# Kernel optimization log

Hardware: AMD Instinct MI355X
Metric: run time of the kernel (lower is better)

The kernel has to match this reference:

```python
import jax, jax.numpy as jnp
import numpy as np

T_MAX = 20
NUM_HEADS = 8
COMPLEXITY_W = 0.3
LN_EPS = 1e-5


def _layernorm(h, g, b):
    mu = jnp.mean(h, axis=-1, keepdims=True)
    var = jnp.var(h, axis=-1, keepdims=True)
    return (h - mu) / jnp.sqrt(var + LN_EPS) * g + b


def _gate_mlp(x, W1, b1, g, be, W2, b2, W3, b3):
    # Linear -> LayerNorm -> ReLU -> (Dropout=id in eval) -> Linear -> ReLU -> Linear -> Sigmoid
    h = jax.nn.relu(_layernorm(x @ W1 + b1, g, be))
    h = jax.nn.relu(h @ W2 + b2)
    return jax.nn.sigmoid(h @ W3 + b3)


def _adaptive_windows(x, p):
    S = x.shape[1]
    gate = _gate_mlp(x, p['gW1'], p['gb1'], p['gg'], p['gbe'], p['gW2'], p['gb2'], p['gW3'], p['gb3'])
    comp = _gate_mlp(x, p['cW1'], p['cb1'], p['cg'], p['cbe'], p['cW2'], p['cb2'], p['cW3'], p['cb3'])
    pos = jnp.linspace(0.8, 1.2, S, dtype=x.dtype).reshape(1, -1, 1)
    score = ((1.0 - COMPLEXITY_W) * gate + COMPLEXITY_W * comp) * pos
    T_i = jnp.clip(jnp.ceil(score[..., 0] * T_MAX), 1, T_MAX).astype(jnp.int32)  # [B,S]
    return T_i


def _spike_sum(x, T_i, alpha, beta):
    # LIF recurrence over T_MAX steps; accumulate masked spikes. x: [B,S,E]
    z = jnp.zeros_like(x)

    def step(carry, t):
        v, i, acc = carry
        active = (t < T_i).astype(x.dtype)[..., None]  # [B,S,1]
        i = alpha * i + x * active
        v = beta * v + i
        s = (v >= 1.0).astype(x.dtype)
        v = v * (1.0 - s)  # v_reset = 0
        return (v, i, acc + s * active), None

    (_, _, acc), _ = jax.lax.scan(step, (z, z, z), jnp.arange(T_MAX))
    return acc


def _forward(x, params):
    B, S, E = x.shape
    H, D = NUM_HEADS, E // NUM_HEADS
    q = x @ params['Wq']
    k = x @ params['Wk']
    v = x @ params['Wv']
    T_i = _adaptive_windows(x, params)
    q_sum = _spike_sum(q, T_i, params['alpha_q'], params['beta_q'])
    k_sum = _spike_sum(k, T_i, params['alpha_k'], params['beta_k'])
    v_mean = _spike_sum(v, T_i, params['alpha_v'], params['beta_v']) / T_MAX
    q_sum = q_sum.reshape(B, S, H, D)
    k_sum = k_sum.reshape(B, S, H, D)
    v_mean = v_mean.reshape(B, S, H, D)
    scale = D ** -0.5
    scores = jnp.einsum('bihd,bjhd->bhij', q_sum, k_sum) * scale
    w = jax.nn.softmax(scores, axis=-1)
    out = jnp.einsum('bhij,bjhd->bihd', w, v_mean).reshape(B, S, E)
    return out @ params['Wo'] + params['bo']


def setup_inputs() -> dict:
    key = jax.random.key(0)
    ks = iter(jax.random.split(key, 32))
    B, S, E = 4, 1024, 512
    f32 = jnp.float32

    def w(shape, scale=0.02):
        return jax.random.normal(next(ks), shape, dtype=f32) * scale

    inp = {
        'x': jax.random.normal(next(ks), (B, S, E), dtype=f32),
        'Wq': w((E, E)), 'Wk': w((E, E)), 'Wv': w((E, E)),
        'Wo': w((E, E)), 'bo': jnp.zeros((E,), f32),
        'gW1': w((E, 128)), 'gb1': jnp.zeros((128,), f32),
        'gg': jnp.ones((128,), f32), 'gbe': jnp.zeros((128,), f32),
        'gW2': w((128, 64)), 'gb2': jnp.zeros((64,), f32),
        'gW3': w((64, 1)), 'gb3': jnp.zeros((1,), f32),
        'cW1': w((E, 64)), 'cb1': jnp.zeros((64,), f32),
        'cg': jnp.ones((64,), f32), 'cbe': jnp.zeros((64,), f32),
        'cW2': w((64, 32)), 'cb2': jnp.zeros((32,), f32),
        'cW3': w((32, 1)), 'cb3': jnp.zeros((1,), f32),
        'alpha_q': jnp.asarray(np.exp(-1 / 5.0), f32), 'beta_q': jnp.asarray(np.exp(-1 / 20.0), f32),
        'alpha_k': jnp.asarray(np.exp(-1 / 5.0), f32), 'beta_k': jnp.asarray(np.exp(-1 / 20.0), f32),
        'alpha_v': jnp.asarray(np.exp(-1 / 5.0), f32), 'beta_v': jnp.asarray(np.exp(-1 / 20.0), f32),
    }
    return inp


def reference(x, Wq, Wk, Wv, Wo, bo,
              gW1, gb1, gg, gbe, gW2, gb2, gW3, gb3,
              cW1, cb1, cg, cbe, cW2, cb2, cW3, cb3,
              alpha_q, beta_q, alpha_k, beta_k, alpha_v, beta_v):
    params = dict(Wq=Wq, Wk=Wk, Wv=Wv, Wo=Wo, bo=bo,
                  gW1=gW1, gb1=gb1, gg=gg, gbe=gbe, gW2=gW2, gb2=gb2, gW3=gW3, gb3=gb3,
                  cW1=cW1, cb1=cb1, cg=cg, cbe=cbe, cW2=cW2, cb2=cb2, cW3=cW3, cb3=cb3,
                  alpha_q=alpha_q, beta_q=beta_q, alpha_k=alpha_k, beta_k=beta_k,
                  alpha_v=alpha_v, beta_v=beta_v)
    return _forward(x, params)
```

## Files before the change

kernel.cpp:

```cpp
#include <hip/hip_runtime.h>
#include <math.h>

#define SEQ   1024
#define EMB   512
#define NROWS 4096
#define LDP   72
#define GROWS 4

typedef __attribute__((ext_vector_type(8))) short short8;
typedef __attribute__((ext_vector_type(4))) float float4v;

__device__ __forceinline__ float bf2f(unsigned short s) {
    union { float f; unsigned u; } x; x.u = ((unsigned)s) << 16; return x.f;
}
__device__ __forceinline__ unsigned short f2bf(float f) {
    union { float f; unsigned u; } x; x.f = f;
    unsigned r = x.u + 0x7fffu + ((x.u >> 16) & 1u);
    return (unsigned short)(r >> 16);
}

__device__ __forceinline__ void split3(float x, unsigned short& h, unsigned short& m, unsigned short& l) {
    union { float f; unsigned u; } a; a.f = x;
    const unsigned rh = a.u + 0x7fffu + ((a.u >> 16) & 1u);
    h = (unsigned short)(rh >> 16);
    union { float f; unsigned u; } hf; hf.u = rh & 0xffff0000u;
    const float r1 = x - hf.f;
    a.f = r1;
    const unsigned rm = a.u + 0x7fffu + ((a.u >> 16) & 1u);
    m = (unsigned short)(rm >> 16);
    union { float f; unsigned u; } mf; mf.u = rm & 0xffff0000u;
    const float r2 = r1 - mf.f;
    l = f2bf(r2);
}

template<int H1, int H2>
__device__ __forceinline__ double gate_mlp_block(
    const double xs[GROWS][EMB], double h1[GROWS][128], double h2[GROWS][64],
    double* red, double* mu_s, double* var_s,
    const float* __restrict__ W1, const float* __restrict__ b1,
    const float* __restrict__ gam, const float* __restrict__ bet,
    const float* __restrict__ W2, const float* __restrict__ b2,
    const float* __restrict__ W3, const float* __restrict__ b3,
    int tid, int myrow)
{
    constexpr int S  = 256 / H1;
    constexpr int KS = EMB / S;

    {
        const int col = tid % H1, sk = tid / H1;
        double acc[GROWS] = {0.0, 0.0, 0.0, 0.0};
        const int kbeg = sk * KS;
        #pragma unroll 4
        for (int k = kbeg; k < kbeg + KS; ++k) {
            const double w = (double)W1[k * H1 + col];
            #pragma unroll
            for (int r = 0; r < GROWS; ++r) acc[r] += w * xs[r][k];
        }
        #pragma unroll
        for (int r = 0; r < GROWS; ++r) red[(sk * GROWS + r) * H1 + col] = acc[r];
    }
    __syncthreads();
    for (int idx = tid; idx < GROWS * H1; idx += 256) {
        const int r = idx / H1, cc = idx % H1;
        double s = 0.0;
        #pragma unroll
        for (int t = 0; t < S; ++t) s += red[(t * GROWS + r) * H1 + cc];
        h1[r][cc] = s + (double)b1[cc];
    }
    __syncthreads();

    {
        const int w = tid >> 6, l = tid & 63;
        double s = 0.0;
        for (int c = l; c < H1; c += 64) s += h1[w][c];
        #pragma unroll
        for (int off = 32; off >= 1; off >>= 1) s += __shfl_xor(s, off);
        if (l == 0) mu_s[w] = s / (double)H1;
    }
    __syncthreads();
    {
        const int w = tid >> 6, l = tid & 63;
        const double mu = mu_s[w];
        double s = 0.0;
        for (int c = l; c < H1; c += 64) { const double d = h1[w][c] - mu; s += d * d; }
        #pragma unroll
        for (int off = 32; off >= 1; off >>= 1) s += __shfl_xor(s, off);
        if (l == 0) var_s[w] = s / (double)H1;
    }
    __syncthreads();
    for (int idx = tid; idx < GROWS * H1; idx += 256) {
        const int r = idx / H1, cc = idx % H1;
        double hn = (h1[r][cc] - mu_s[r]) / sqrt(var_s[r] + 1e-5) * (double)gam[cc] + (double)bet[cc];
        h1[r][cc] = hn > 0.0 ? hn : 0.0;
    }
    __syncthreads();

    {
        const int col = tid % H2;
        const int r   = tid / H2;
        if (r < GROWS) {
            double acc = (double)b2[col];
            for (int k = 0; k < H1; ++k)
                acc += (double)W2[k * H2 + col] * h1[r][k];
            h2[r][col] = acc > 0.0 ? acc : 0.0;
        }
    }
    __syncthreads();

    {
        const int w = tid >> 6, l = tid & 63;
        double s = 0.0;
        for (int c = l; c < H2; c += 64) s += h2[w][c] * (double)W3[c];
        #pragma unroll
        for (int off = 32; off >= 1; off >>= 1) s += __shfl_xor(s, off);
        if (l == 0) mu_s[w] = s;
    }
    __syncthreads();
    double ret = 0.0;
    if (myrow >= 0) {
        const double z = mu_s[myrow] + (double)b3[0];
        ret = 1.0 / (1.0 + exp(-z));
    }
    __syncthreads();
    return ret;
}

__global__ __launch_bounds__(256) void gates_kernel(
    const float* __restrict__ x,
    const float* __restrict__ gW1, const float* __restrict__ gb1,
    const float* __restrict__ gg,  const float* __restrict__ gbe,
    const float* __restrict__ gW2, const float* __restrict__ gb2,
    const float* __restrict__ gW3, const float* __restrict__ gb3,
    const float* __restrict__ cW1, const float* __restrict__ cb1,
    const float* __restrict__ cg,  const float* __restrict__ cbe,
    const float* __restrict__ cW2, const float* __restrict__ cb2,
    const float* __restrict__ cW3, const float* __restrict__ cb3,
    int* __restrict__ T_i)
{
    __shared__ double xs[GROWS][EMB];
    __shared__ double h1[GROWS][128];
    __shared__ double h2[GROWS][64];
    __shared__ double red[1024];
    __shared__ double mu_s[GROWS], var_s[GROWS];

    const int row0 = blockIdx.x * GROWS;
    const int tid = threadIdx.x;

    for (int idx = tid; idx < GROWS * EMB; idx += 256) {
        const int r = idx >> 9, cc = idx & 511;
        xs[r][cc] = (double)x[(size_t)(row0 + r) * EMB + cc];
    }
    __syncthreads();

    const int myrow = (tid < GROWS) ? tid : -1;
    const double g0 = gate_mlp_block<128, 64>(xs, h1, h2, red, mu_s, var_s,
                                              gW1, gb1, gg, gbe, gW2, gb2, gW3, gb3, tid, myrow);
    const double c0 = gate_mlp_block<64, 32>(xs, h1, h2, red, mu_s, var_s,
                                             cW1, cb1, cg, cbe, cW2, cb2, cW3, cb3, tid, myrow);

    if (tid < GROWS) {
        const int row = row0 + tid;
        const int s = row & (SEQ - 1);
        const double step = (1.2 - 0.8) / (double)(SEQ - 1);
        const double pos  = (double)s * step + 0.8;
        const double score = ((1.0 - 0.3) * g0 + 0.3 * c0) * pos;
        double t = ceil(score * 20.0);
        t = t < 1.0 ? 1.0 : (t > 20.0 ? 20.0 : t);
        T_i[row] = (int)t;
    }
}

__global__ __launch_bounds__(256) void w_limbs_prep(
    const float* __restrict__ Wq, const float* __restrict__ Wk, const float* __restrict__ Wv,
    unsigned short* __restrict__ WL)
{
    const int z = blockIdx.z;
    const float* __restrict__ W = (z == 0) ? Wq : (z == 1) ? Wk : Wv;
    unsigned short* __restrict__ Th = WL + (size_t)z * 3 * EMB * EMB;
    unsigned short* __restrict__ Tm = Th + (size_t)EMB * EMB;
    unsigned short* __restrict__ Tl = Tm + (size_t)EMB * EMB;

    __shared__ __align__(16) float Ws[64][68];
    const int k0 = blockIdx.y * 64, n0 = blockIdx.x * 64;
    const int t = threadIdx.x;
    #pragma unroll
    for (int it = 0; it < 4; ++it) {
        const int idx = it * 256 + t;
        const int r = idx >> 4, c4 = (idx & 15) * 4;
        *(float4*)&Ws[r][c4] = *(const float4*)&W[(size_t)(k0 + r) * EMB + n0 + c4];
    }
    __syncthreads();
    #pragma unroll
    for (int it = 0; it < 2; ++it) {
        const int idx = it * 256 + t;
        const int n = idx >> 3, k8 = (idx & 7) * 8;
        short8 ph, pm, pl;
        #pragma unroll
        for (int j = 0; j < 8; ++j) {
            unsigned short h, m, l;
            split3(Ws[k8 + j][n], h, m, l);
            ph[j] = (short)h; pm[j] = (short)m; pl[j] = (short)l;
        }
        const size_t o = (size_t)(n0 + n) * EMB + k0 + k8;
        *(short8*)&Th[o] = ph;
        *(short8*)&Tm[o] = pm;
        *(short8*)&Tl[o] = pl;
    }
}

__global__ __launch_bounds__(256) void x_limbs_prep(
    const float* __restrict__ x, unsigned short* __restrict__ XL)
{
    unsigned short* __restrict__ Xh = XL;
    unsigned short* __restrict__ Xm = XL + (size_t)NROWS * EMB;
    unsigned short* __restrict__ Xl = Xm + (size_t)NROWS * EMB;
    const size_t i0 = ((size_t)blockIdx.x * 256 + threadIdx.x) * 8;
    const float4 a0 = *(const float4*)&x[i0];
    const float4 a1 = *(const float4*)&x[i0 + 4];
    const float av8[8] = {a0.x, a0.y, a0.z, a0.w, a1.x, a1.y, a1.z, a1.w};
    short8 ph, pm, pl;
    #pragma unroll
    for (int e = 0; e < 8; ++e) {
        unsigned short h, m, l;
        split3(av8[e], h, m, l);
        ph[e] = (short)h; pm[e] = (short)m; pl[e] = (short)l;
    }
    *(short8*)&Xh[i0] = ph;
    *(short8*)&Xm[i0] = pm;
    *(short8*)&Xl[i0] = pl;
}

__global__ __launch_bounds__(256) void qkv_mfma_lif_kernel(
    const unsigned short* __restrict__ XL, const unsigned short* __restrict__ WL,
    const float* __restrict__ aq, const float* __restrict__ bq,
    const float* __restrict__ akp, const float* __restrict__ bkp,
    const float* __restrict__ av, const float* __restrict__ bv,
    const int* __restrict__ T_i,
    unsigned short* __restrict__ q_sum, unsigned short* __restrict__ k_sum,
    unsigned short* __restrict__ v_mean)
{
    const int z = blockIdx.z;
    const unsigned short* __restrict__ WTh = WL + (size_t)z * 3 * EMB * EMB;
    const unsigned short* __restrict__ WTm = WTh + (size_t)EMB * EMB;
    const unsigned short* __restrict__ WTl = WTm + (size_t)EMB * EMB;
    const unsigned short* __restrict__ Xh = XL;
    const unsigned short* __restrict__ Xm = XL + (size_t)NROWS * EMB;
    const unsigned short* __restrict__ Xl = Xm + (size_t)NROWS * EMB;
    unsigned short* __restrict__ out = (z == 0) ? q_sum : (z == 1) ? k_sum : v_mean;
    const double alpha = (double)((z == 0) ? aq : (z == 1) ? akp : av)[0];
    const double beta  = (double)((z == 0) ? bq : (z == 1) ? bkp : bv)[0];

    const int phys = blockIdx.x + 8 * blockIdx.y;
    const int logical = (phys & 7) * 32 + (phys >> 3);
    const int bx = logical & 7, by = logical >> 3;
    const int row0 = by * 128, col0 = bx * 64;

    __shared__ __align__(16) short As[3][128 * 32];
    __shared__ __align__(16) short Bs[3][64 * 32];

    const int tid  = threadIdx.x;
    const int lane = tid & 63, wave = tid >> 6;
    const int qd = lane >> 4, c = lane & 15;
    const int wrow = wave * 32;

    const int ar  = tid >> 1, akc = (tid & 1) * 2;
    const int br  = tid >> 2, bkc = tid & 3;
    const size_t aio = (size_t)(row0 + ar) * EMB + akc * 8;
    const size_t bio = (size_t)(col0 + br) * EMB + bkc * 8;
    const int asw = (ar >> 1) & 3, bsw = (br >> 1) & 3;
    const int ad0 = ar * 32 + ((akc ^ asw) * 8);
    const int ad1 = ar * 32 + (((akc + 1) ^ asw) * 8);
    const int bd  = br * 32 + ((bkc ^ bsw) * 8);

    int arf[2], brf[4];
    #pragma unroll
    for (int i = 0; i < 2; ++i) {
        const int Ra = wrow + i * 16 + c;
        arf[i] = Ra * 32 + ((qd ^ ((Ra >> 1) & 3)) * 8);
    }
    #pragma unroll
    for (int j = 0; j < 4; ++j) {
        const int Rb = j * 16 + c;
        brf[j] = Rb * 32 + ((qd ^ ((Rb >> 1) & 3)) * 8);
    }

    float4v acc[2][4];
    #pragma unroll
    for (int i = 0; i < 2; ++i)
        #pragma unroll
        for (int j = 0; j < 4; ++j)
            acc[i][j] = (float4v){0.f, 0.f, 0.f, 0.f};

    for (int k0 = 0; k0 < EMB; k0 += 32) {
        const short8 ah0 = *(const short8*)&Xh[aio + k0];
        const short8 ah1 = *(const short8*)&Xh[aio + k0 + 8];
        const short8 am0 = *(const short8*)&Xm[aio + k0];
        const short8 am1 = *(const short8*)&Xm[aio + k0 + 8];
        const short8 al0 = *(const short8*)&Xl[aio + k0];
        const short8 al1 = *(const short8*)&Xl[aio + k0 + 8];
        const short8 bh  = *(const short8*)&WTh[bio + k0];
        const short8 bm  = *(const short8*)&WTm[bio + k0];
        const short8 bl  = *(const short8*)&WTl[bio + k0];

        __syncthreads();
        *(short8*)&As[0][ad0] = ah0; *(short8*)&As[0][ad1] = ah1;
        *(short8*)&As[1][ad0] = am0; *(short8*)&As[1][ad1] = am1;
        *(short8*)&As[2][ad0] = al0; *(short8*)&As[2][ad1] = al1;
        *(short8*)&Bs[0][bd] = bh;
        *(short8*)&Bs[1][bd] = bm;
        *(short8*)&Bs[2][bd] = bl;
        __syncthreads();

        short8 Afh[2], Afm[2], Afl[2];
        #pragma unroll
        for (int i = 0; i < 2; ++i) {
            Afh[i] = *(const short8*)&As[0][arf[i]];
            Afm[i] = *(const short8*)&As[1][arf[i]];
            Afl[i] = *(const short8*)&As[2][arf[i]];
        }
        short8 Bfh[4], Bfm[4], Bfl[4];
        #pragma unroll
        for (int j = 0; j < 4; ++j) {
            Bfh[j] = *(const short8*)&Bs[0][brf[j]];
            Bfm[j] = *(const short8*)&Bs[1][brf[j]];
            Bfl[j] = *(const short8*)&Bs[2][brf[j]];
        }

        #pragma unroll
        for (int i = 0; i < 2; ++i)
            #pragma unroll
            for (int j = 0; j < 4; ++j) {
                float4v t = acc[i][j];
                t = __builtin_amdgcn_mfma_f32_16x16x32_bf16(Afh[i], Bfh[j], t, 0, 0, 0);
                t = __builtin_amdgcn_mfma_f32_16x16x32_bf16(Afh[i], Bfm[j], t, 0, 0, 0);
                t = __builtin_amdgcn_mfma_f32_16x16x32_bf16(Afm[i], Bfh[j], t, 0, 0, 0);
                t = __builtin_amdgcn_mfma_f32_16x16x32_bf16(Afm[i], Bfm[j], t, 0, 0, 0);
                t = __builtin_amdgcn_mfma_f32_16x16x32_bf16(Afh[i], Bfl[j], t, 0, 0, 0);
                t = __builtin_amdgcn_mfma_f32_16x16x32_bf16(Afl[i], Bfh[j], t, 0, 0, 0);
                acc[i][j] = t;
            }
    }

    #pragma unroll
    for (int i = 0; i < 2; ++i)
        #pragma unroll
        for (int r = 0; r < 4; ++r) {
            const int gm = row0 + wrow + i * 16 + qd * 4 + r;
            const int T = T_i[gm];
            double cur0 = 0.0, cur1 = 0.0, cur2 = 0.0, cur3 = 0.0;
            double vm0 = 0.0, vm1 = 0.0, vm2 = 0.0, vm3 = 0.0;
            double sp0 = 0.0, sp1 = 0.0, sp2 = 0.0, sp3 = 0.0;
            const double xv0 = (double)acc[i][0][r];
            const double xv1 = (double)acc[i][1][r];
            const double xv2 = (double)acc[i][2][r];
            const double xv3 = (double)acc[i][3][r];
            for (int t = 0; t < T; ++t) {
                cur0 = alpha * cur0 + xv0; vm0 = beta * vm0 + cur0;
                if (vm0 >= 1.0) { sp0 += 1.0; vm0 = 0.0; }
                cur1 = alpha * cur1 + xv1; vm1 = beta * vm1 + cur1;
                if (vm1 >= 1.0) { sp1 += 1.0; vm1 = 0.0; }
                cur2 = alpha * cur2 + xv2; vm2 = beta * vm2 + cur2;
                if (vm2 >= 1.0) { sp2 += 1.0; vm2 = 0.0; }
                cur3 = alpha * cur3 + xv3; vm3 = beta * vm3 + cur3;
                if (vm3 >= 1.0) { sp3 += 1.0; vm3 = 0.0; }
            }
            if (z == 2) { sp0 /= 20.0; sp1 /= 20.0; sp2 /= 20.0; sp3 /= 20.0; }
            const size_t ob = (size_t)gm * EMB + col0 + c;
            out[ob +  0] = f2bf((float)sp0);
            out[ob + 16] = f2bf((float)sp1);
            out[ob + 32] = f2bf((float)sp2);
            out[ob + 48] = f2bf((float)sp3);
        }
}

__global__ __launch_bounds__(256) void attn_mfma_kernel(
    const unsigned short* __restrict__ q, const unsigned short* __restrict__ k,
    const unsigned short* __restrict__ v, unsigned short* __restrict__ attn_bf)
{
    __shared__ __align__(16) short Ks[64 * LDP];
    __shared__ __align__(16) short Pt[64 * LDP];
    __shared__ __align__(16) short Vt[64 * LDP];

    const int b = blockIdx.z, h = blockIdx.y;
    const int i0 = blockIdx.x * 64;
    const int tid  = threadIdx.x;
    const int wave = tid >> 6, lane = tid & 63;
    const int quad = lane >> 4, c = lane & 15;

    const unsigned short* Qb = q + ((size_t)b * SEQ + i0) * EMB + h * 64;
    const unsigned short* Kb = k + (size_t)b * SEQ * EMB + h * 64;
    const unsigned short* Vb = v + (size_t)b * SEQ * EMB + h * 64;

    short8 qf[2];
    {
        const int qrow = wave * 16 + c;
        #pragma unroll
        for (int ks = 0; ks < 2; ++ks) {
            short8 raw = *(const short8*)(Qb + (size_t)qrow * EMB + ks * 32 + quad * 8);
            short8 sc8;
            #pragma unroll
            for (int j = 0; j < 8; ++j)
                sc8[j] = (short)f2bf(bf2f((unsigned short)raw[j]) * 0.125f);
            qf[ks] = sc8;
        }
    }

    float m_r[4], l_r[4];
    float4v o[4];
    #pragma unroll
    for (int r = 0; r < 4; ++r) { m_r[r] = -1e30f; l_r[r] = 0.f; }
    #pragma unroll
    for (int nb = 0; nb < 4; ++nb)
        #pragma unroll
        for (int r = 0; r < 4; ++r) o[nb][r] = 0.f;

    for (int jt = 0; jt < SEQ / 64; ++jt) {
        #pragma unroll
        for (int it = 0; it < 2; ++it) {
            const int idx = it * 256 + tid;
            const int row = idx >> 3, ch = idx & 7;
            short8 val = *(const short8*)(Kb + (size_t)(jt * 64 + row) * EMB + ch * 8);
            *(short8*)&Ks[row * LDP + ch * 8] = val;
        }
        __syncthreads();

        float sc[4][4];
        #pragma unroll
        for (int nb = 0; nb < 4; ++nb) {
            float4v acc = {0.f, 0.f, 0.f, 0.f};
            #pragma unroll
            for (int ks = 0; ks < 2; ++ks) {
                short8 bfrag = *(const short8*)&Ks[(nb * 16 + c) * LDP + ks * 32 + quad * 8];
                acc = __builtin_amdgcn_mfma_f32_16x16x32_bf16(qf[ks], bfrag, acc, 0, 0, 0);
            }
            #pragma unroll
            for (int r = 0; r < 4; ++r) sc[nb][r] = acc[r];
        }

        float mnew[4], alpha[4];
        #pragma unroll
        for (int r = 0; r < 4; ++r) {
            float mx = fmaxf(fmaxf(sc[0][r], sc[1][r]), fmaxf(sc[2][r], sc[3][r]));
            #pragma unroll
            for (int off = 8; off >= 1; off >>= 1) mx = fmaxf(mx, __shfl_xor(mx, off));
            mnew[r]  = fmaxf(m_r[r], mx);
            alpha[r] = __expf(m_r[r] - mnew[r]);
            m_r[r]   = mnew[r];
        }
        float psum[4] = {0.f, 0.f, 0.f, 0.f};
        #pragma unroll
        for (int nb = 0; nb < 4; ++nb)
            #pragma unroll
            for (int r = 0; r < 4; ++r) {
                float p = __expf(sc[nb][r] - mnew[r]);
                psum[r] += p;
                Pt[(wave * 16 + quad * 4 + r) * LDP + nb * 16 + c] = (short)f2bf(p);
            }
        #pragma unroll
        for (int r = 0; r < 4; ++r) {
            float s = psum[r];
            #pragma unroll
            for (int off = 8; off >= 1; off >>= 1) s += __shfl_xor(s, off);
            l_r[r] = l_r[r] * alpha[r] + s;
            #pragma unroll
            for (int nb = 0; nb < 4; ++nb) o[nb][r] *= alpha[r];
        }

        {
            const int m = tid & 7, rp = tid >> 3;
            const int r = rp * 2;
            short8 v0 = *(const short8*)(Vb + (size_t)(jt * 64 + r) * EMB + m * 8);
            short8 v1 = *(const short8*)(Vb + (size_t)(jt * 64 + r + 1) * EMB + m * 8);
            const int rch = r >> 3, rlow = r & 7;
            #pragma unroll
            for (int i = 0; i < 8; ++i) {
                const int d = m * 8 + i;
                const int col = ((rch ^ m) << 3) + rlow;
                *(int*)&Vt[d * LDP + col] =
                    (int)((unsigned)(unsigned short)v0[i] |
                          ((unsigned)(unsigned short)v1[i] << 16));
            }
        }
        __syncthreads();

        short8 pf[2];
        #pragma unroll
        for (int ks = 0; ks < 2; ++ks)
            pf[ks] = *(const short8*)&Pt[(wave * 16 + c) * LDP + ks * 32 + quad * 8];
        #pragma unroll
        for (int nb = 0; nb < 4; ++nb) {
            float4v acc = o[nb];
            #pragma unroll
            for (int ks = 0; ks < 2; ++ks) {
                const int d = nb * 16 + c;
                const int kch = ks * 4 + quad;
                const int col = ((kch ^ (d >> 3)) << 3);
                short8 vfrag = *(const short8*)&Vt[d * LDP + col];
                acc = __builtin_amdgcn_mfma_f32_16x16x32_bf16(pf[ks], vfrag, acc, 0, 0, 0);
            }
            o[nb] = acc;
        }
    }

    #pragma unroll
    for (int r = 0; r < 4; ++r) {
        const float inv = 1.0f / l_r[r];
        const int row = i0 + wave * 16 + quad * 4 + r;
        #pragma unroll
        for (int nb = 0; nb < 4; ++nb)
            attn_bf[((size_t)b * SEQ + row) * EMB + h * 64 + nb * 16 + c] =
                f2bf(o[nb][r] * inv);
    }
}

__global__ __launch_bounds__(256) void wot_prep(
    const float* __restrict__ Wo, unsigned short* __restrict__ BT)
{
    __shared__ unsigned short Ws[64][72];
    const int k0 = blockIdx.y * 64, n0 = blockIdx.x * 64;
    const int t = threadIdx.x;
    #pragma unroll
    for (int it = 0; it < 4; ++it) {
        const int idx = it * 256 + t;
        const int r = idx >> 4, c4 = (idx & 15) * 4;
        const float4 w4 = *(const float4*)&Wo[(size_t)(k0 + r) * EMB + n0 + c4];
        Ws[r][c4 + 0] = f2bf(w4.x); Ws[r][c4 + 1] = f2bf(w4.y);
        Ws[r][c4 + 2] = f2bf(w4.z); Ws[r][c4 + 3] = f2bf(w4.w);
    }
    __syncthreads();
    #pragma unroll
    for (int it = 0; it < 2; ++it) {
        const int idx = it * 256 + t;
        const int n = idx >> 3, k8 = (idx & 7) * 8;
        short8 pack;
        #pragma unroll
        for (int j = 0; j < 8; ++j) pack[j] = (short)Ws[k8 + j][n];
        *(short8*)&BT[(size_t)(n0 + n) * EMB + k0 + k8] = pack;
    }
}

__global__ __launch_bounds__(256) void out_gemm_kernel(
    const unsigned short* __restrict__ A,
    const unsigned short* __restrict__ BT,
    const float* __restrict__ bias, float* __restrict__ out)
{
    const int tid  = threadIdx.x;
    const int lane = tid & 63, wave = tid >> 6;
    const int qd = lane >> 4, c = lane & 15;
    const int wm = (wave & 1) * 32, wn = (wave >> 1) * 32;
    const int row0 = blockIdx.y * 64, col0 = blockIdx.x * 64;

    float4v acc[2][2];
    #pragma unroll
    for (int i = 0; i < 2; ++i)
        #pragma unroll
        for (int j = 0; j < 2; ++j)
            acc[i][j] = (float4v){0.f, 0.f, 0.f, 0.f};

    for (int k0 = 0; k0 < EMB; k0 += 32) {
        short8 af[2], bf[2];
        #pragma unroll
        for (int i = 0; i < 2; ++i)
            af[i] = *(const short8*)&A[(size_t)(row0 + wm + i * 16 + c) * EMB + k0 + qd * 8];
        #pragma unroll
        for (int j = 0; j < 2; ++j)
            bf[j] = *(const short8*)&BT[(size_t)(col0 + wn + j * 16 + c) * EMB + k0 + qd * 8];
        #pragma unroll
        for (int i = 0; i < 2; ++i)
            #pragma unroll
            for (int j = 0; j < 2; ++j)
                acc[i][j] = __builtin_amdgcn_mfma_f32_16x16x32_bf16(af[i], bf[j], acc[i][j], 0, 0, 0);
    }

    #pragma unroll
    for (int i = 0; i < 2; ++i)
        #pragma unroll
        for (int r = 0; r < 4; ++r) {
            const int gm = row0 + wm + i * 16 + qd * 4 + r;
            #pragma unroll
            for (int j = 0; j < 2; ++j) {
                const int gn = col0 + wn + j * 16 + c;
                out[(size_t)gm * EMB + gn] = acc[i][j][r] + bias[gn];
            }
        }
}

extern "C" void kernel_launch(void* const* d_in, const int* in_sizes, int n_in,
                              void* d_out, int out_size, void* d_ws, size_t ws_size,
                              hipStream_t stream)
{
    const float* x   = (const float*)d_in[0];
    const float* Wq  = (const float*)d_in[1];
    const float* Wk  = (const float*)d_in[2];
    const float* Wv  = (const float*)d_in[3];
    const float* Wo  = (const float*)d_in[4];
    const float* bo  = (const float*)d_in[5];
    const float* gW1 = (const float*)d_in[6];
    const float* gb1 = (const float*)d_in[7];
    const float* gg  = (const float*)d_in[8];
    const float* gbe = (const float*)d_in[9];
    const float* gW2 = (const float*)d_in[10];
    const float* gb2 = (const float*)d_in[11];
    const float* gW3 = (const float*)d_in[12];
    const float* gb3 = (const float*)d_in[13];
    const float* cW1 = (const float*)d_in[14];
    const float* cb1 = (const float*)d_in[15];
    const float* cg  = (const float*)d_in[16];
    const float* cbe = (const float*)d_in[17];
    const float* cW2 = (const float*)d_in[18];
    const float* cb2 = (const float*)d_in[19];
    const float* cW3 = (const float*)d_in[20];
    const float* cb3 = (const float*)d_in[21];
    const float* aq  = (const float*)d_in[22];
    const float* bq  = (const float*)d_in[23];
    const float* ak  = (const float*)d_in[24];
    const float* bk  = (const float*)d_in[25];
    const float* av  = (const float*)d_in[26];
    const float* bv  = (const float*)d_in[27];

    int* Tp = (int*)d_ws;
    unsigned short* q_sum   = (unsigned short*)((char*)d_ws + 16384);
    unsigned short* k_sum   = q_sum   + (size_t)NROWS * EMB;
    unsigned short* v_mean  = k_sum   + (size_t)NROWS * EMB;
    unsigned short* attn_bf = v_mean  + (size_t)NROWS * EMB;
    unsigned short* WoT     = attn_bf + (size_t)NROWS * EMB;
    unsigned short* WL      = WoT     + (size_t)EMB * EMB;
    unsigned short* XLp     = WL      + (size_t)9 * EMB * EMB;
    float* out = (float*)d_out;

    gates_kernel<<<dim3(NROWS / GROWS), dim3(256), 0, stream>>>(
        x, gW1, gb1, gg, gbe, gW2, gb2, gW3, gb3,
        cW1, cb1, cg, cbe, cW2, cb2, cW3, cb3, Tp);

    x_limbs_prep<<<dim3(NROWS * EMB / (256 * 8)), dim3(256), 0, stream>>>(x, XLp);

    w_limbs_prep<<<dim3(EMB / 64, EMB / 64, 3), dim3(256), 0, stream>>>(Wq, Wk, Wv, WL);

    qkv_mfma_lif_kernel<<<dim3(EMB / 64, NROWS / 128, 3), dim3(256), 0, stream>>>(
        XLp, WL, aq, bq, ak, bk, av, bv, Tp, q_sum, k_sum, v_mean);

    wot_prep<<<dim3(EMB / 64, EMB / 64), dim3(256), 0, stream>>>(Wo, WoT);

    attn_mfma_kernel<<<dim3(SEQ / 64, 8, 4), dim3(256), 0, stream>>>(
        q_sum, k_sum, v_mean, attn_bf);

    out_gemm_kernel<<<dim3(EMB / 64, NROWS / 64), dim3(256), 0, stream>>>(
        attn_bf, WoT, bo, out);
}
```

Measured before the change: 271.6 us.

## Split gate MLPs across blocks and use direct global-to-LDS loads in QKV GEMM

The gate and complexity MLPs now run in separate blocks along a second grid dimension, each writing a double score to workspace. A new small kernel combines the two scores into T_i. The first-layer reduction is restructured so each thread handles whole rows without the shared split-K buffer. Separately, the QKV MFMA kernel stages its A/B tiles with global_load_lds (direct-to-LDS) using a new swizzle, instead of going through registers. These changes raise parallelism in the gate stage and cut register traffic in the GEMM, at the cost of an extra launch and a workspace buffer. Each gate thread now runs a serial loop over the full K of 512 with four accumulators, which lengthens per-thread latency.

After: 287.5 us. 5.8% more time.

```diff
diff --git a/kernel.cpp b/kernel.cpp
--- a/kernel.cpp
+++ b/kernel.cpp
@@ -17,6 +17,12 @@
     union { float f; unsigned u; } x; x.f = f;
     unsigned r = x.u + 0x7fffu + ((x.u >> 16) & 1u);
     return (unsigned short)(r >> 16);
+}
+
+__device__ __forceinline__ void gld16(const unsigned short* g, short* l) {
+    __builtin_amdgcn_global_load_lds(
+        (__attribute__((address_space(1))) void*)(g),
+        (__attribute__((address_space(3))) void*)(l), 16, 0, 0);
 }
 
 __device__ __forceinline__ void split3(float x, unsigned short& h, unsigned short& m, unsigned short& l) {
@@ -34,45 +40,39 @@
 }
 
 template<int H1, int H2>
-__device__ __forceinline__ double gate_mlp_block(
-    const double xs[GROWS][EMB], double h1[GROWS][128], double h2[GROWS][64],
-    double* red, double* mu_s, double* var_s,
+__device__ __forceinline__ double mlp_eval(
+    const double xs[GROWS][EMB], double* h1, double* h2,
+    double* mu_s, double* var_s,
     const float* __restrict__ W1, const float* __restrict__ b1,
     const float* __restrict__ gam, const float* __restrict__ bet,
     const float* __restrict__ W2, const float* __restrict__ b2,
     const float* __restrict__ W3, const float* __restrict__ b3,
     int tid, int myrow)
 {
-    constexpr int S  = 256 / H1;
-    constexpr int KS = EMB / S;
+    constexpr int RPT = GROWS * H1 / 256;
 
     {
-        const int col = tid % H1, sk = tid / H1;
-        double acc[GROWS] = {0.0, 0.0, 0.0, 0.0};
-        const int kbeg = sk * KS;
-        #pragma unroll 4
-        for (int k = kbeg; k < kbeg + KS; ++k) {
-            const double w = (double)W1[k * H1 + col];
-            #pragma unroll
-            for (int r = 0; r < GROWS; ++r) acc[r] += w * xs[r][k];
-        }
-        #pragma unroll
-        for (int r = 0; r < GROWS; ++r) red[(sk * GROWS + r) * H1 + col] = acc[r];
-    }
-    __syncthreads();
-    for (int idx = tid; idx < GROWS * H1; idx += 256) {
-        const int r = idx / H1, cc = idx % H1;
-        double s = 0.0;
-        #pragma unroll
-        for (int t = 0; t < S; ++t) s += red[(t * GROWS + r) * H1 + cc];
-        h1[r][cc] = s + (double)b1[cc];
+        const int col = tid % H1;
+        const int r0  = (tid / H1) * RPT;
+        #pragma unroll
+        for (int rr = 0; rr < RPT; ++rr) {
+            const double* xr = xs[r0 + rr];
+            double a0 = 0.0, a1 = 0.0, a2 = 0.0, a3 = 0.0;
+            for (int k = 0; k < EMB; k += 4) {
+                a0 += (double)W1[(k + 0) * H1 + col] * xr[k + 0];
+                a1 += (double)W1[(k + 1) * H1 + col] * xr[k + 1];
+                a2 += (double)W1[(k + 2) * H1 + col] * xr[k + 2];
+                a3 += (double)W1[(k + 3) * H1 + col] * xr[k + 3];
+            }
+            h1[(r0 + rr) * H1 + col] = ((a0 + a1) + (a2 + a3)) + (double)b1[col];
+        }
     }
     __syncthreads();
 
     {
         const int w = tid >> 6, l = tid & 63;
         double s = 0.0;
-        for (int c = l; c < H1; c += 64) s += h1[w][c];
+        for (int c = l; c < H1; c += 64) s += h1[w * H1 + c];
         #pragma unroll
         for (int off = 32; off >= 1; off >>= 1) s += __shfl_xor(s, off);
         if (l == 0) mu_s[w] = s / (double)H1;
@@ -82,7 +82,7 @@
         const int w = tid >> 6, l = tid & 63;
         const double mu = mu_s[w];
         double s = 0.0;
-        for (int c = l; c < H1; c += 64) { const double d = h1[w][c] - mu; s += d * d; }
+        for (int c = l; c < H1; c += 64) { const double d = h1[w * H1 + c] - mu; s += d * d; }
         #pragma unroll
         for (int off = 32; off >= 1; off >>= 1) s += __shfl_xor(s, off);
         if (l == 0) var_s[w] = s / (double)H1;
@@ -90,8 +90,8 @@
     __syncthreads();
     for (int idx = tid; idx < GROWS * H1; idx += 256) {
         const int r = idx / H1, cc = idx % H1;
-        double hn = (h1[r][cc] - mu_s[r]) / sqrt(var_s[r] + 1e-5) * (double)gam[cc] + (double)bet[cc];
-        h1[r][cc] = hn > 0.0 ? hn : 0.0;
+        double hn = (h1[r * H1 + cc] - mu_s[r]) / sqrt(var_s[r] + 1e-5) * (double)gam[cc] + (double)bet[cc];
+        h1[r * H1 + cc] = hn > 0.0 ? hn : 0.0;
     }
     __syncthreads();
 
@@ -101,8 +101,8 @@
         if (r < GROWS) {
             double acc = (double)b2[col];
             for (int k = 0; k < H1; ++k)
-                acc += (double)W2[k * H2 + col] * h1[r][k];
-            h2[r][col] = acc > 0.0 ? acc : 0.0;
+                acc += (double)W2[k * H2 + col] * h1[r * H1 + k];
+            h2[r * H2 + col] = acc > 0.0 ? acc : 0.0;
         }
     }
     __syncthreads();
@@ -110,7 +110,7 @@
     {
         const int w = tid >> 6, l = tid & 63;
         double s = 0.0;
-        for (int c = l; c < H2; c += 64) s += h2[w][c] * (double)W3[c];
+        for (int c = l; c < H2; c += 64) s += h2[w * H2 + c] * (double)W3[c];
         #pragma unroll
         for (int off = 32; off >= 1; off >>= 1) s += __shfl_xor(s, off);
         if (l == 0) mu_s[w] = s;
@@ -121,11 +121,10 @@
         const double z = mu_s[myrow] + (double)b3[0];
         ret = 1.0 / (1.0 + exp(-z));
     }
-    __syncthreads();
     return ret;
 }
 
-__global__ __launch_bounds__(256) void gates_kernel(
+__global__ __launch_bounds__(256) void gates_split_kernel(
     const float* __restrict__ x,
     const float* __restrict__ gW1, const float* __restrict__ gb1,
     const float* __restrict__ gg,  const float* __restrict__ gbe,
@@ -135,12 +134,11 @@
     const float* __restrict__ cg,  const float* __restrict__ cbe,
     const float* __restrict__ cW2, const float* __restrict__ cb2,
     const float* __restrict__ cW3, const float* __restrict__ cb3,
-    int* __restrict__ T_i)
+    double* __restrict__ scores)
 {
     __shared__ double xs[GROWS][EMB];
-    __shared__ double h1[GROWS][128];
-    __shared__ double h2[GROWS][64];
-    __shared__ double red[1024];
+    __shared__ double h1[GROWS * 128];
+    __shared__ double h2[GROWS * 64];
     __shared__ double mu_s[GROWS], var_s[GROWS];
 
     const int row0 = blockIdx.x * GROWS;
@@ -153,21 +151,31 @@
     __syncthreads();
 
     const int myrow = (tid < GROWS) ? tid : -1;
-    const double g0 = gate_mlp_block<128, 64>(xs, h1, h2, red, mu_s, var_s,
-                                              gW1, gb1, gg, gbe, gW2, gb2, gW3, gb3, tid, myrow);
-    const double c0 = gate_mlp_block<64, 32>(xs, h1, h2, red, mu_s, var_s,
-                                             cW1, cb1, cg, cbe, cW2, cb2, cW3, cb3, tid, myrow);
-
-    if (tid < GROWS) {
-        const int row = row0 + tid;
-        const int s = row & (SEQ - 1);
-        const double step = (1.2 - 0.8) / (double)(SEQ - 1);
-        const double pos  = (double)s * step + 0.8;
-        const double score = ((1.0 - 0.3) * g0 + 0.3 * c0) * pos;
-        double t = ceil(score * 20.0);
-        t = t < 1.0 ? 1.0 : (t > 20.0 ? 20.0 : t);
-        T_i[row] = (int)t;
-    }
+    double v;
+    if (blockIdx.y == 0)
+        v = mlp_eval<128, 64>(xs, h1, h2, mu_s, var_s,
+                              gW1, gb1, gg, gbe, gW2, gb2, gW3, gb3, tid, myrow);
+    else
+        v = mlp_eval<64, 32>(xs, h1, h2, mu_s, var_s,
+                             cW1, cb1, cg, cbe, cW2, cb2, cW3, cb3, tid, myrow);
+
+    if (myrow >= 0)
+        scores[(size_t)blockIdx.y * NROWS + row0 + myrow] = v;
+}
+
+__global__ __launch_bounds__(256) void tcomb_kernel(
+    const double* __restrict__ scores, int* __restrict__ T_i)
+{
+    const int row = blockIdx.x * 256 + threadIdx.x;
+    const double g0 = scores[row];
+    const double c0 = scores[NROWS + row];
+    const int s = row & (SEQ - 1);
+    const double step = (1.2 - 0.8) / (double)(SEQ - 1);
+    const double pos  = (double)s * step + 0.8;
+    const double score = ((1.0 - 0.3) * g0 + 0.3 * c0) * pos;
+    double t = ceil(score * 20.0);
+    t = t < 1.0 ? 1.0 : (t > 20.0 ? 20.0 : t);
+    T_i[row] = (int)t;
 }
 
 __global__ __launch_bounds__(256) void w_limbs_prep(
@@ -263,14 +271,10 @@
     const int qd = lane >> 4, c = lane & 15;
     const int wrow = wave * 32;
 
-    const int ar  = tid >> 1, akc = (tid & 1) * 2;
-    const int br  = tid >> 2, bkc = tid & 3;
-    const size_t aio = (size_t)(row0 + ar) * EMB + akc * 8;
-    const size_t bio = (size_t)(col0 + br) * EMB + bkc * 8;
-    const int asw = (ar >> 1) & 3, bsw = (br >> 1) & 3;
-    const int ad0 = ar * 32 + ((akc ^ asw) * 8);
-    const int ad1 = ar * 32 + (((akc + 1) ^ asw) * 8);
-    const int bd  = br * 32 + ((bkc ^ bsw) * 8);
+    const int kc8 = ((lane & 3) ^ ((lane >> 3) & 3)) * 8;
+    const size_t ga0 = (size_t)(row0 + wave * 16 + (lane >> 2)) * EMB + kc8;
+    const size_t ga1 = ga0 + (size_t)64 * EMB;
+    const size_t gb  = (size_t)(col0 + wave * 16 + (lane >> 2)) * EMB + kc8;
 
     int arf[2], brf[4];
     #pragma unroll
@@ -292,23 +296,16 @@
             acc[i][j] = (float4v){0.f, 0.f, 0.f, 0.f};
 
     for (int k0 = 0; k0 < EMB; k0 += 32) {
-        const short8 ah0 = *(const short8*)&Xh[aio + k0];
-        const short8 ah1 = *(const short8*)&Xh[aio + k0 + 8];
-        const short8 am0 = *(const short8*)&Xm[aio + k0];
-        const short8 am1 = *(const short8*)&Xm[aio + k0 + 8];
-        const short8 al0 = *(const short8*)&Xl[aio + k0];
-        const short8 al1 = *(const short8*)&Xl[aio + k0 + 8];
-        const short8 bh  = *(const short8*)&WTh[bio + k0];
-        const short8 bm  = *(const short8*)&WTm[bio + k0];
-        const short8 bl  = *(const short8*)&WTl[bio + k0];
-
         __syncthreads();
-        *(short8*)&As[0][ad0] = ah0; *(short8*)&As[0][ad1] = ah1;
-        *(short8*)&As[1][ad0] = am0; *(short8*)&As[1][ad1] = am1;
-        *(short8*)&As[2][ad0] = al0; *(short8*)&As[2][ad1] = al1;
-        *(short8*)&Bs[0][bd] = bh;
-        *(short8*)&Bs[1][bd] = bm;
-        *(short8*)&Bs[2][bd] = bl;
+        gld16(Xh  + ga0 + k0, &As[0][wave * 512]);
+        gld16(Xh  + ga1 + k0, &As[0][2048 + wave * 512]);
+        gld16(Xm  + ga0 + k0, &As[1][wave * 512]);
+        gld16(Xm  + ga1 + k0, &As[1][2048 + wave * 512]);
+        gld16(Xl  + ga0 + k0, &As[2][wave * 512]);
+        gld16(Xl  + ga1 + k0, &As[2][2048 + wave * 512]);
+        gld16(WTh + gb  + k0, &Bs[0][wave * 512]);
+        gld16(WTm + gb  + k0, &Bs[1][wave * 512]);
+        gld16(WTl + gb  + k0, &Bs[2][wave * 512]);
         __syncthreads();
 
         short8 Afh[2], Afm[2], Afl[2];
@@ -626,15 +623,18 @@
     unsigned short* WoT     = attn_bf + (size_t)NROWS * EMB;
     unsigned short* WL      = WoT     + (size_t)EMB * EMB;
     unsigned short* XLp     = WL      + (size_t)9 * EMB * EMB;
+    double* scores          = (double*)(XLp + (size_t)3 * NROWS * EMB);
     float* out = (float*)d_out;
 
-    gates_kernel<<<dim3(NROWS / GROWS), dim3(256), 0, stream>>>(
+    gates_split_kernel<<<dim3(NROWS / GROWS, 2), dim3(256), 0, stream>>>(
         x, gW1, gb1, gg, gbe, gW2, gb2, gW3, gb3,
-        cW1, cb1, cg, cbe, cW2, cb2, cW3, cb3, Tp);
+        cW1, cb1, cg, cbe, cW2, cb2, cW3, cb3, scores);
 
     x_limbs_prep<<<dim3(NROWS * EMB / (256 * 8)), dim3(256), 0, stream>>>(x, XLp);
 
     w_limbs_prep<<<dim3(EMB / 64, EMB / 64, 3), dim3(256), 0, stream>>>(Wq, Wk, Wv, WL);
+
+    tcomb_kernel<<<dim3(NROWS / 256), dim3(256), 0, stream>>>(scores, Tp);
 
     qkv_mfma_lif_kernel<<<dim3(EMB / 64, NROWS / 128, 3), dim3(256), 0, stream>>>(
         XLp, WL, aq, bq, ak, bk, av, bv, Tp, q_sum, k_sum, v_mean);
```
